# Performance work log

Measured on AMD Instinct MI355X. Metric: run time of the kernel, lower is better.

The kernel has to match this reference:

```python
import jax, jax.numpy as jnp
import numpy as np

NQ = 8
DIM = 2 ** NQ  # 256
PAIRS = [(i, j) for i in range(NQ) for j in range(i + 1, NQ)]
CNOT = jnp.array([[1, 0, 0, 0], [0, 1, 0, 0], [0, 0, 0, 1], [0, 0, 1, 0]], jnp.complex64)


def rx(t):
    c = jnp.cos(t / 2).astype(jnp.complex64)
    s = (-1j * jnp.sin(t / 2)).astype(jnp.complex64)
    return jnp.stack([jnp.stack([c, s]), jnp.stack([s, c])])


def ry(t):
    c = jnp.cos(t / 2)
    s = jnp.sin(t / 2)
    return jnp.stack([jnp.stack([c, -s]), jnp.stack([s, c])]).astype(jnp.complex64)


def rz(t):
    e = jnp.exp(-1j * jnp.asarray(t, jnp.float32) / 2).astype(jnp.complex64)
    z = jnp.zeros((), jnp.complex64)
    return jnp.stack([jnp.stack([e, z]), jnp.stack([z, jnp.conj(e)])])


def ising_xx(phi):
    c = jnp.cos(phi / 2).astype(jnp.complex64)
    s = (-1j * jnp.sin(phi / 2)).astype(jnp.complex64)
    z = jnp.zeros((), jnp.complex64)
    return jnp.stack([
        jnp.stack([c, z, z, s]),
        jnp.stack([z, c, s, z]),
        jnp.stack([z, s, c, z]),
        jnp.stack([s, z, z, c]),
    ])


def apply_u(rho, U, wires):
    """rho: (2,)*16 tensor (8 ket axes, 8 bra axes). Apply U rho U^dagger on wires."""
    k = len(wires)
    Ut = U.reshape((2,) * (2 * k))
    rho = jnp.tensordot(Ut, rho, axes=(tuple(range(k, 2 * k)), tuple(wires)))
    rho = jnp.moveaxis(rho, tuple(range(k)), tuple(wires))
    bra = tuple(w + NQ for w in wires)
    rho = jnp.tensordot(jnp.conj(Ut), rho, axes=(tuple(range(k, 2 * k)), bra))
    rho = jnp.moveaxis(rho, tuple(range(k)), bra)
    return rho


def conv_block(rho, b1, b2, p):
    rho = apply_u(rho, rz(-jnp.pi / 2), (b2,))
    rho = apply_u(rho, CNOT, (b2, b1))
    rho = apply_u(rho, rz(p[0]), (b1,))
    rho = apply_u(rho, ry(p[1]), (b2,))
    rho = apply_u(rho, CNOT, (b1, b2))
    rho = apply_u(rho, ry(p[2]), (b2,))
    rho = apply_u(rho, CNOT, (b2, b1))
    rho = apply_u(rho, rz(jnp.pi / 2), (b1,))
    return rho


def pool_block(rho, b1, b2, p):
    rho = apply_u(rho, rz(-jnp.pi / 2), (b2,))
    rho = apply_u(rho, CNOT, (b2, b1))
    rho = apply_u(rho, rz(p[0]), (b1,))
    rho = apply_u(rho, ry(p[1]), (b2,))
    rho = apply_u(rho, CNOT, (b1, b2))
    rho = apply_u(rho, ry(p[2]), (b2,))
    return rho


def quantum_fusion_layer(x, weights, coupling, p_flip):
    # AmplitudeEmbedding with normalize=True -> pure state, then rho = |psi><psi|
    psi = (x / jnp.sqrt(jnp.sum(x * x))).astype(jnp.complex64)
    rho = jnp.outer(psi, jnp.conj(psi)).reshape((2,) * (2 * NQ))
    X = jnp.array([[0, 1], [1, 0]], jnp.complex64)
    for i in range(NQ):
        rho = apply_u(rho, rx(weights[i]), (i,))
        rho = apply_u(rho, ry(weights[i + NQ]), (i,))
        rho = apply_u(rho, rz(weights[i + 2 * NQ]), (i,))
        if p_flip > 0.0:  # BitFlip channel; identity when p=0
            rho = (1.0 - p_flip) * rho + p_flip * apply_u(rho, X, (i,))
    for (i, j) in PAIRS:
        rho = apply_u(rho, ising_xx(coupling[i, j]), (i, j))
    # data-dependent adjacency -> blend (equivalent to conditional apply for adj in {0,1})
    cmin = coupling.min()
    cmax = coupling.max()
    adj = ((coupling - cmin) / (cmax - cmin)) > 0.5
    count = jnp.zeros((), jnp.int32)
    for (i, j) in PAIRS:
        a = adj[i, j]
        idx = 3 * NQ + 6 * count
        p6 = jax.lax.dynamic_slice(weights, (idx,), (6,))
        r2 = conv_block(rho, i, j, p6[:3])
        r2 = pool_block(r2, i, j, p6[3:])
        af = a.astype(jnp.float32)
        rho = af * r2 + (1.0 - af) * rho
        count = count + a.astype(jnp.int32)
    return rho.reshape(DIM, DIM)


def setup_inputs() -> dict:
    key = jax.random.key(0)
    k1, k2, k3 = jax.random.split(key, 3)
    x = jax.random.uniform(k1, (DIM,), dtype=jnp.float32)
    weights = jax.random.uniform(k2, (210,), dtype=jnp.float32)
    coupling = jax.random.uniform(k3, (NQ, NQ), dtype=jnp.float32)
    return {"x": x, "weights": weights, "coupling": coupling}


def reference(x, weights, coupling):
    # forward returns the noiseless state (noise_strength=0); the noisy run is only printed
    return quantum_fusion_layer(x, weights, coupling, 0.0)
```

## Files before the change

kernel.cpp:

```cpp
#include <hip/hip_runtime.h>

#define RHALF 0.70710678118654752440f

struct St { float vr[4]; float vi[4]; int lane; };

static __device__ __forceinline__ void phase_mul(float& ar, float& ai, float c, float s) {
    float nr = c*ar - s*ai;
    float ni = c*ai + s*ar;
    ar = nr; ai = ni;
}

static __device__ __forceinline__ void xxupd(float& ar, float& ai, float pr, float pi, float c, float s) {
    ar = c*ar + s*pi;
    ai = c*ai - s*pr;
}

static __device__ __forceinline__ void rx_pair(float& ar, float& ai, float& br, float& bi, float c, float s) {
    float nar = c*ar + s*bi, nai = c*ai - s*br;
    float nbr = c*br + s*ai, nbi = c*bi - s*ar;
    ar=nar; ai=nai; br=nbr; bi=nbi;
}

static __device__ __forceinline__ void ry_pair(float& ar, float& ai, float& br, float& bi, float c, float s) {
    float nar = c*ar - s*br, nai = c*ai - s*bi;
    float nbr = s*ar + c*br, nbi = s*ai + c*bi;
    ar=nar; ai=nai; br=nbr; bi=nbi;
}

static __device__ __forceinline__ void cswap2(float& ar, float& ai, float& br, float& bi, bool ctl) {
    float n0 = ctl ? br : ar, n1 = ctl ? ar : br;
    float m0 = ctl ? bi : ai, m1 = ctl ? ai : bi;
    ar = n0; br = n1; ai = m0; bi = m1;
}

static __device__ __forceinline__ void swapf(float& a, float& b) { float t=a; a=b; b=t; }

static __device__ __forceinline__ void xx2(float& ar,float& ai,float& br,float& bi,int lm,float c,float s) {
    float pbr = __shfl_xor(ar, lm, 64), pbi = __shfl_xor(ai, lm, 64);
    float par = __shfl_xor(br, lm, 64), pai = __shfl_xor(bi, lm, 64);
    xxupd(ar,ai,par,pai,c,s);
    xxupd(br,bi,pbr,pbi,c,s);
}


static __device__ __forceinline__ void gRZ(St& st, int q, float c, float s) {
    if (q == 0) {
        phase_mul(st.vr[0],st.vi[0],c,-s); phase_mul(st.vr[1],st.vi[1],c,-s);
        phase_mul(st.vr[2],st.vi[2],c, s); phase_mul(st.vr[3],st.vi[3],c, s);
    } else if (q == 1) {
        phase_mul(st.vr[0],st.vi[0],c,-s); phase_mul(st.vr[2],st.vi[2],c,-s);
        phase_mul(st.vr[1],st.vi[1],c, s); phase_mul(st.vr[3],st.vi[3],c, s);
    } else {
        int ml = 1 << (7-q);
        float sg = (st.lane & ml) ? s : -s;
        phase_mul(st.vr[0],st.vi[0],c,sg);
        phase_mul(st.vr[1],st.vi[1],c,sg);
        phase_mul(st.vr[2],st.vi[2],c,sg);
        phase_mul(st.vr[3],st.vi[3],c,sg);
    }
}

static __device__ __forceinline__ void gRX(St& st, int q, float c, float s) {
    if (q == 0) {
        rx_pair(st.vr[0],st.vi[0],st.vr[2],st.vi[2],c,s);
        rx_pair(st.vr[1],st.vi[1],st.vr[3],st.vi[3],c,s);
    } else if (q == 1) {
        rx_pair(st.vr[0],st.vi[0],st.vr[1],st.vi[1],c,s);
        rx_pair(st.vr[2],st.vi[2],st.vr[3],st.vi[3],c,s);
    } else {
        int ml = 1 << (7-q);
        #pragma unroll
        for (int k=0;k<4;++k) {
            float pr = __shfl_xor(st.vr[k], ml, 64);
            float pi = __shfl_xor(st.vi[k], ml, 64);
            xxupd(st.vr[k], st.vi[k], pr, pi, c, s);
        }
    }
}

static __device__ __forceinline__ void gRY(St& st, int q, float c, float s) {
    if (q == 0) {
        ry_pair(st.vr[0],st.vi[0],st.vr[2],st.vi[2],c,s);
        ry_pair(st.vr[1],st.vi[1],st.vr[3],st.vi[3],c,s);
    } else if (q == 1) {
        ry_pair(st.vr[0],st.vi[0],st.vr[1],st.vi[1],c,s);
        ry_pair(st.vr[2],st.vi[2],st.vr[3],st.vi[3],c,s);
    } else {
        int ml = 1 << (7-q);
        float pc = (st.lane & ml) ? s : -s;
        #pragma unroll
        for (int k=0;k<4;++k) {
            float pr = __shfl_xor(st.vr[k], ml, 64);
            float pi = __shfl_xor(st.vi[k], ml, 64);
            st.vr[k] = c*st.vr[k] + pc*pr;
            st.vi[k] = c*st.vi[k] + pc*pi;
        }
    }
}

static __device__ __forceinline__ void gCNOT(St& st, int qc, int qt) {
    if (qc <= 1 && qt <= 1) {
        if (qc == 0) { swapf(st.vr[2],st.vr[3]); swapf(st.vi[2],st.vi[3]); }
        else         { swapf(st.vr[1],st.vr[3]); swapf(st.vi[1],st.vi[3]); }
    } else if (qc <= 1) {
        int ml = 1 << (7-qt);
        if (qc == 0) {
            st.vr[2]=__shfl_xor(st.vr[2],ml,64); st.vi[2]=__shfl_xor(st.vi[2],ml,64);
            st.vr[3]=__shfl_xor(st.vr[3],ml,64); st.vi[3]=__shfl_xor(st.vi[3],ml,64);
        } else {
            st.vr[1]=__shfl_xor(st.vr[1],ml,64); st.vi[1]=__shfl_xor(st.vi[1],ml,64);
            st.vr[3]=__shfl_xor(st.vr[3],ml,64); st.vi[3]=__shfl_xor(st.vi[3],ml,64);
        }
    } else if (qt <= 1) {
        int mlc = 1 << (7-qc);
        bool ctl = (st.lane & mlc) != 0;
        if (qt == 0) {
            cswap2(st.vr[0],st.vi[0],st.vr[2],st.vi[2],ctl);
            cswap2(st.vr[1],st.vi[1],st.vr[3],st.vi[3],ctl);
        } else {
            cswap2(st.vr[0],st.vi[0],st.vr[1],st.vi[1],ctl);
            cswap2(st.vr[2],st.vi[2],st.vr[3],st.vi[3],ctl);
        }
    } else {
        int mlt = 1 << (7-qt);
        int mlc = 1 << (7-qc);
        bool ctl = (st.lane & mlc) != 0;
        #pragma unroll
        for (int k=0;k<4;++k) {
            float pr = __shfl_xor(st.vr[k], mlt, 64);
            float pi = __shfl_xor(st.vi[k], mlt, 64);
            st.vr[k] = ctl ? pr : st.vr[k];
            st.vi[k] = ctl ? pi : st.vi[k];
        }
    }
}

static __device__ __forceinline__ void gXX(St& st, int qa, int qb, float c, float s) {
    if (qb <= 1) {
        float p0r=st.vr[3],p0i=st.vi[3],p1r=st.vr[2],p1i=st.vi[2];
        float p2r=st.vr[1],p2i=st.vi[1],p3r=st.vr[0],p3i=st.vi[0];
        xxupd(st.vr[0],st.vi[0],p0r,p0i,c,s);
        xxupd(st.vr[1],st.vi[1],p1r,p1i,c,s);
        xxupd(st.vr[2],st.vi[2],p2r,p2i,c,s);
        xxupd(st.vr[3],st.vi[3],p3r,p3i,c,s);
    } else if (qa <= 1) {
        int lm = 1 << (7-qb);
        if (qa == 0) {
            xx2(st.vr[0],st.vi[0],st.vr[2],st.vi[2],lm,c,s);
            xx2(st.vr[1],st.vi[1],st.vr[3],st.vi[3],lm,c,s);
        } else {
            xx2(st.vr[0],st.vi[0],st.vr[1],st.vi[1],lm,c,s);
            xx2(st.vr[2],st.vi[2],st.vr[3],st.vi[3],lm,c,s);
        }
    } else {
        int lm = (1<<(7-qa)) | (1<<(7-qb));
        #pragma unroll
        for (int k=0;k<4;++k) {
            float pr = __shfl_xor(st.vr[k], lm, 64);
            float pi = __shfl_xor(st.vi[k], lm, 64);
            xxupd(st.vr[k],st.vi[k],pr,pi,c,s);
        }
    }
}

__global__ __launch_bounds__(64) void evolve_kernel(const float* __restrict__ x,
                                                    const float* __restrict__ w,
                                                    const float* __restrict__ cp,
                                                    float2* __restrict__ psi) {
    __shared__ float2 tw[256];
    __shared__ float2 tc[64];
    int lane = threadIdx.x;

    #pragma unroll
    for (int k=0;k<4;++k) {
        int idx = k*64 + lane;
        float a = (idx < 210) ? w[idx] : 0.0f;
        float sn, cn; sincosf(0.5f*a, &sn, &cn);
        tw[idx] = make_float2(cn, sn);
    }
    float cv = cp[lane];
    { float sn, cn; sincosf(0.5f*cv, &sn, &cn); tc[lane] = make_float2(cn, sn); }

    St st; st.lane = lane;
    float ss = 0.f;
    #pragma unroll
    for (int k=0;k<4;++k) {
        float xv = x[k*64 + lane];
        st.vr[k] = xv; st.vi[k] = 0.f;
        ss += xv*xv;
    }
    #pragma unroll
    for (int m=32;m>0;m>>=1) ss += __shfl_xor(ss, m, 64);
    float inv = 1.0f / sqrtf(ss);
    #pragma unroll
    for (int k=0;k<4;++k) st.vr[k] *= inv;

    float mn = cv, mx = cv;
    #pragma unroll
    for (int m=32;m>0;m>>=1) {
        mn = fminf(mn, __shfl_xor(mn, m, 64));
        mx = fmaxf(mx, __shfl_xor(mx, m, 64));
    }
    unsigned long long adj = __ballot(((cv - mn) / (mx - mn)) > 0.5f);

    __syncthreads();

    #pragma unroll
    for (int q=0;q<8;++q) {
        float2 cs;
        cs = tw[q];      gRX(st, q, cs.x, cs.y);
        cs = tw[q+8];    gRY(st, q, cs.x, cs.y);
        cs = tw[q+16];   gRZ(st, q, cs.x, cs.y);
    }

    #pragma unroll
    for (int i=0;i<8;++i) {
        #pragma unroll
        for (int j=i+1;j<8;++j) {
            float2 cs = tc[i*8+j];
            gXX(st, i, j, cs.x, cs.y);
        }
    }

    int count = 0;
    #pragma unroll
    for (int i=0;i<8;++i) {
        #pragma unroll
        for (int j=i+1;j<8;++j) {
            if ((adj >> (i*8 + j)) & 1ull) {
                int pb = 24 + 6*count;
                float2 cs;
                gRZ(st, j, RHALF, -RHALF);
                gCNOT(st, j, i);
                cs = tw[pb+0]; gRZ(st, i, cs.x, cs.y);
                cs = tw[pb+1]; gRY(st, j, cs.x, cs.y);
                gCNOT(st, i, j);
                cs = tw[pb+2]; gRY(st, j, cs.x, cs.y);
                gCNOT(st, j, i);
                gRZ(st, i, RHALF, RHALF);
                gRZ(st, j, RHALF, -RHALF);
                gCNOT(st, j, i);
                cs = tw[pb+3]; gRZ(st, i, cs.x, cs.y);
                cs = tw[pb+4]; gRY(st, j, cs.x, cs.y);
                gCNOT(st, i, j);
                cs = tw[pb+5]; gRY(st, j, cs.x, cs.y);
                ++count;
            }
        }
    }

    #pragma unroll
    for (int k=0;k<4;++k) psi[k*64+lane] = make_float2(st.vr[k], st.vi[k]);
}

__global__ __launch_bounds__(256) void outer_planar(const float2* __restrict__ psi,
                                                    float* __restrict__ out) {
    int c = threadIdx.x;
    int r = blockIdx.x;
    float2 pr = psi[r];
    float2 pc = psi[c];
    int idx = (r<<8) + c;
    out[idx]         = pr.x*pc.x + pr.y*pc.y;
    out[idx + 65536] = pr.y*pc.x - pr.x*pc.y;
}

__global__ __launch_bounds__(256) void outer_real(const float2* __restrict__ psi,
                                                  float* __restrict__ out) {
    int c = threadIdx.x;
    int r = blockIdx.x;
    float2 pr = psi[r];
    float2 pc = psi[c];
    out[(r<<8) + c] = pr.x*pc.x + pr.y*pc.y;
}

__global__ __launch_bounds__(256) void outer_interleaved(const float2* __restrict__ psi,
                                                         float2* __restrict__ out) {
    int c = threadIdx.x;
    int r = blockIdx.x;
    float2 pr = psi[r];
    float2 pc = psi[c];
    out[(r<<8) + c] = make_float2(pr.x*pc.x + pr.y*pc.y, pr.y*pc.x - pr.x*pc.y);
}

extern "C" void kernel_launch(void* const* d_in, const int* in_sizes, int n_in,
                              void* d_out, int out_size, void* d_ws, size_t ws_size,
                              hipStream_t stream) {
    (void)in_sizes; (void)n_in; (void)ws_size;
    const float* x  = (const float*)d_in[0];
    const float* w  = (const float*)d_in[1];
    const float* cp = (const float*)d_in[2];
    float2* psi = (float2*)d_ws;
    hipLaunchKernelGGL(evolve_kernel, dim3(1), dim3(64), 0, stream, x, w, cp, psi);
    if (out_size == 65536) {
        hipLaunchKernelGGL(outer_real, dim3(256), dim3(256), 0, stream, psi, (float*)d_out);
    } else if (out_size == 131072) {
        hipLaunchKernelGGL(outer_planar, dim3(256), dim3(256), 0, stream, psi, (float*)d_out);
    } else {
        hipLaunchKernelGGL(outer_interleaved, dim3(256), dim3(256), 0, stream, psi, (float2*)d_out);
    }
}
```

Measured before the change: 73.98 us.

## Precompute fused 4x4 two-qubit block unitaries and fused single-qubit gates

Each conditional conv+pool block, a sequence of CNOT, RZ and RY gates, is collapsed into one 4x4 complex matrix. The 28 lanes build these matrices in parallel and store them in shared memory, and the state is then updated with a single dense two-qubit apply per active pair. The RX, RY and RZ layers on each qubit are likewise fused into one 2x2 unitary. The IsingXX gates are reordered so that consecutive gates mix lanes differently. The goal is fewer sequential shuffle and gate steps on the single-wavefront critical path, at the cost of dense complex MACs and more shuffles per fused block.

Result: faster. 68.14 us (-7.9%).

```diff
diff --git a/kernel.cpp b/kernel.cpp
--- a/kernel.cpp
+++ b/kernel.cpp
@@ -2,38 +2,22 @@
 
 #define RHALF 0.70710678118654752440f
 
+typedef float2 cpx;
+
+static __device__ __forceinline__ cpx cmul(cpx a, cpx b) {
+    return make_float2(a.x*b.x - a.y*b.y, a.x*b.y + a.y*b.x);
+}
+static __device__ __forceinline__ void cmac(cpx& n, cpx k, cpx a) {
+    n.x += k.x*a.x - k.y*a.y;
+    n.y += k.x*a.y + k.y*a.x;
+}
+
 struct St { float vr[4]; float vi[4]; int lane; };
-
-static __device__ __forceinline__ void phase_mul(float& ar, float& ai, float c, float s) {
-    float nr = c*ar - s*ai;
-    float ni = c*ai + s*ar;
-    ar = nr; ai = ni;
-}
 
 static __device__ __forceinline__ void xxupd(float& ar, float& ai, float pr, float pi, float c, float s) {
     ar = c*ar + s*pi;
     ai = c*ai - s*pr;
 }
-
-static __device__ __forceinline__ void rx_pair(float& ar, float& ai, float& br, float& bi, float c, float s) {
-    float nar = c*ar + s*bi, nai = c*ai - s*br;
-    float nbr = c*br + s*ai, nbi = c*bi - s*ar;
-    ar=nar; ai=nai; br=nbr; bi=nbi;
-}
-
-static __device__ __forceinline__ void ry_pair(float& ar, float& ai, float& br, float& bi, float c, float s) {
-    float nar = c*ar - s*br, nai = c*ai - s*bi;
-    float nbr = s*ar + c*br, nbi = s*ai + c*bi;
-    ar=nar; ai=nai; br=nbr; bi=nbi;
-}
-
-static __device__ __forceinline__ void cswap2(float& ar, float& ai, float& br, float& bi, bool ctl) {
-    float n0 = ctl ? br : ar, n1 = ctl ? ar : br;
-    float m0 = ctl ? bi : ai, m1 = ctl ? ai : bi;
-    ar = n0; br = n1; ai = m0; bi = m1;
-}
-
-static __device__ __forceinline__ void swapf(float& a, float& b) { float t=a; a=b; b=t; }
 
 static __device__ __forceinline__ void xx2(float& ar,float& ai,float& br,float& bi,int lm,float c,float s) {
     float pbr = __shfl_xor(ar, lm, 64), pbi = __shfl_xor(ai, lm, 64);
@@ -42,98 +26,6 @@
     xxupd(br,bi,pbr,pbi,c,s);
 }
 
-
-static __device__ __forceinline__ void gRZ(St& st, int q, float c, float s) {
-    if (q == 0) {
-        phase_mul(st.vr[0],st.vi[0],c,-s); phase_mul(st.vr[1],st.vi[1],c,-s);
-        phase_mul(st.vr[2],st.vi[2],c, s); phase_mul(st.vr[3],st.vi[3],c, s);
-    } else if (q == 1) {
-        phase_mul(st.vr[0],st.vi[0],c,-s); phase_mul(st.vr[2],st.vi[2],c,-s);
-        phase_mul(st.vr[1],st.vi[1],c, s); phase_mul(st.vr[3],st.vi[3],c, s);
-    } else {
-        int ml = 1 << (7-q);
-        float sg = (st.lane & ml) ? s : -s;
-        phase_mul(st.vr[0],st.vi[0],c,sg);
-        phase_mul(st.vr[1],st.vi[1],c,sg);
-        phase_mul(st.vr[2],st.vi[2],c,sg);
-        phase_mul(st.vr[3],st.vi[3],c,sg);
-    }
-}
-
-static __device__ __forceinline__ void gRX(St& st, int q, float c, float s) {
-    if (q == 0) {
-        rx_pair(st.vr[0],st.vi[0],st.vr[2],st.vi[2],c,s);
-        rx_pair(st.vr[1],st.vi[1],st.vr[3],st.vi[3],c,s);
-    } else if (q == 1) {
-        rx_pair(st.vr[0],st.vi[0],st.vr[1],st.vi[1],c,s);
-        rx_pair(st.vr[2],st.vi[2],st.vr[3],st.vi[3],c,s);
-    } else {
-        int ml = 1 << (7-q);
-        #pragma unroll
-        for (int k=0;k<4;++k) {
-            float pr = __shfl_xor(st.vr[k], ml, 64);
-            float pi = __shfl_xor(st.vi[k], ml, 64);
-            xxupd(st.vr[k], st.vi[k], pr, pi, c, s);
-        }
-    }
-}
-
-static __device__ __forceinline__ void gRY(St& st, int q, float c, float s) {
-    if (q == 0) {
-        ry_pair(st.vr[0],st.vi[0],st.vr[2],st.vi[2],c,s);
-        ry_pair(st.vr[1],st.vi[1],st.vr[3],st.vi[3],c,s);
-    } else if (q == 1) {
-        ry_pair(st.vr[0],st.vi[0],st.vr[1],st.vi[1],c,s);
-        ry_pair(st.vr[2],st.vi[2],st.vr[3],st.vi[3],c,s);
-    } else {
-        int ml = 1 << (7-q);
-        float pc = (st.lane & ml) ? s : -s;
-        #pragma unroll
-        for (int k=0;k<4;++k) {
-            float pr = __shfl_xor(st.vr[k], ml, 64);
-            float pi = __shfl_xor(st.vi[k], ml, 64);
-            st.vr[k] = c*st.vr[k] + pc*pr;
-            st.vi[k] = c*st.vi[k] + pc*pi;
-        }
-    }
-}
-
-static __device__ __forceinline__ void gCNOT(St& st, int qc, int qt) {
-    if (qc <= 1 && qt <= 1) {
-        if (qc == 0) { swapf(st.vr[2],st.vr[3]); swapf(st.vi[2],st.vi[3]); }
-        else         { swapf(st.vr[1],st.vr[3]); swapf(st.vi[1],st.vi[3]); }
-    } else if (qc <= 1) {
-        int ml = 1 << (7-qt);
-        if (qc == 0) {
-            st.vr[2]=__shfl_xor(st.vr[2],ml,64); st.vi[2]=__shfl_xor(st.vi[2],ml,64);
-            st.vr[3]=__shfl_xor(st.vr[3],ml,64); st.vi[3]=__shfl_xor(st.vi[3],ml,64);
-        } else {
-            st.vr[1]=__shfl_xor(st.vr[1],ml,64); st.vi[1]=__shfl_xor(st.vi[1],ml,64);
-            st.vr[3]=__shfl_xor(st.vr[3],ml,64); st.vi[3]=__shfl_xor(st.vi[3],ml,64);
-        }
-    } else if (qt <= 1) {
-        int mlc = 1 << (7-qc);
-        bool ctl = (st.lane & mlc) != 0;
-        if (qt == 0) {
-            cswap2(st.vr[0],st.vi[0],st.vr[2],st.vi[2],ctl);
-            cswap2(st.vr[1],st.vi[1],st.vr[3],st.vi[3],ctl);
-        } else {
-            cswap2(st.vr[0],st.vi[0],st.vr[1],st.vi[1],ctl);
-            cswap2(st.vr[2],st.vi[2],st.vr[3],st.vi[3],ctl);
-        }
-    } else {
-        int mlt = 1 << (7-qt);
-        int mlc = 1 << (7-qc);
-        bool ctl = (st.lane & mlc) != 0;
-        #pragma unroll
-        for (int k=0;k<4;++k) {
-            float pr = __shfl_xor(st.vr[k], mlt, 64);
-            float pi = __shfl_xor(st.vi[k], mlt, 64);
-            st.vr[k] = ctl ? pr : st.vr[k];
-            st.vi[k] = ctl ? pi : st.vi[k];
-        }
-    }
-}
 
 static __device__ __forceinline__ void gXX(St& st, int qa, int qb, float c, float s) {
     if (qb <= 1) {
@@ -163,23 +55,77 @@
     }
 }
 
+
+static __device__ __forceinline__ void applyBlockLL(St& st, const cpx* bm, int p, int i, int j) {
+    int mi = 1 << (7-i), mj = 1 << (7-j);
+    int r = ((st.lane & mi) ? 2 : 0) | ((st.lane & mj) ? 1 : 0);
+    const cpx* row = bm + p*16 + r*4;
+    cpx K0 = row[r], K1 = row[r^1], K2 = row[r^2], K3 = row[r^3];
+    #pragma unroll
+    for (int k=0;k<4;++k) {
+        float p1r = __shfl_xor(st.vr[k], mj, 64),    p1i = __shfl_xor(st.vi[k], mj, 64);
+        float p2r = __shfl_xor(st.vr[k], mi, 64),    p2i = __shfl_xor(st.vi[k], mi, 64);
+        float p3r = __shfl_xor(st.vr[k], mi|mj, 64), p3i = __shfl_xor(st.vi[k], mi|mj, 64);
+        cpx n = make_float2(0.f,0.f);
+        cmac(n, K0, make_float2(st.vr[k], st.vi[k]));
+        cmac(n, K1, make_float2(p1r,p1i));
+        cmac(n, K2, make_float2(p2r,p2i));
+        cmac(n, K3, make_float2(p3r,p3i));
+        st.vr[k] = n.x; st.vi[k] = n.y;
+    }
+}
+
+static __device__ __forceinline__ void applyBlockMixed(St& st, const cpx* bm, int p, int i, int j) {
+    int mj = 1 << (7-j);
+    int bj = (st.lane & mj) ? 1 : 0;
+    const cpx* base = bm + p*16;
+    cpx lo0 = base[bj*4+0], lo1 = base[bj*4+1], lo2 = base[bj*4+2], lo3 = base[bj*4+3];
+    cpx hi0 = base[(2+bj)*4+0], hi1 = base[(2+bj)*4+1], hi2 = base[(2+bj)*4+2], hi3 = base[(2+bj)*4+3];
+    cpx lo_o0 = bj ? lo1 : lo0;  cpx lo_s0 = bj ? lo0 : lo1;
+    cpx lo_o1 = bj ? lo3 : lo2;  cpx lo_s1 = bj ? lo2 : lo3;
+    cpx hi_o0 = bj ? hi1 : hi0;  cpx hi_s0 = bj ? hi0 : hi1;
+    cpx hi_o1 = bj ? hi3 : hi2;  cpx hi_s1 = bj ? hi2 : hi3;
+    float sr[4], si[4];
+    #pragma unroll
+    for (int k=0;k<4;++k) { sr[k] = __shfl_xor(st.vr[k], mj, 64); si[k] = __shfl_xor(st.vi[k], mj, 64); }
+    int ri = (i==0) ? 2 : 1;
+    #pragma unroll
+    for (int t=0; t<2; ++t) {
+        int k0 = (i==0) ? t : (t*2);
+        int k1 = k0 | ri;
+        cpx a0 = make_float2(st.vr[k0], st.vi[k0]);
+        cpx a1 = make_float2(st.vr[k1], st.vi[k1]);
+        cpx s0 = make_float2(sr[k0], si[k0]);
+        cpx s1 = make_float2(sr[k1], si[k1]);
+        cpx n0 = make_float2(0.f,0.f), n1 = make_float2(0.f,0.f);
+        cmac(n0, lo_o0, a0); cmac(n0, lo_s0, s0); cmac(n0, lo_o1, a1); cmac(n0, lo_s1, s1);
+        cmac(n1, hi_o0, a0); cmac(n1, hi_s0, s0); cmac(n1, hi_o1, a1); cmac(n1, hi_s1, s1);
+        st.vr[k0]=n0.x; st.vi[k0]=n0.y; st.vr[k1]=n1.x; st.vi[k1]=n1.y;
+    }
+}
+
+static __device__ __forceinline__ void applyBlock01(St& st, const cpx* bm, int p) {
+    const cpx* base = bm + p*16;
+    cpx a[4];
+    #pragma unroll
+    for (int k=0;k<4;++k) a[k] = make_float2(st.vr[k], st.vi[k]);
+    #pragma unroll
+    for (int r=0;r<4;++r) {
+        cpx n = make_float2(0.f,0.f);
+        #pragma unroll
+        for (int c=0;c<4;++c) cmac(n, base[r*4+c], a[c]);
+        st.vr[r]=n.x; st.vi[r]=n.y;
+    }
+}
+
 __global__ __launch_bounds__(64) void evolve_kernel(const float* __restrict__ x,
                                                     const float* __restrict__ w,
                                                     const float* __restrict__ cp,
                                                     float2* __restrict__ psi) {
-    __shared__ float2 tw[256];
-    __shared__ float2 tc[64];
+    __shared__ cpx tc[64];
+    __shared__ cpx u1[32];
+    __shared__ cpx bmat[28*16];
     int lane = threadIdx.x;
-
-    #pragma unroll
-    for (int k=0;k<4;++k) {
-        int idx = k*64 + lane;
-        float a = (idx < 210) ? w[idx] : 0.0f;
-        float sn, cn; sincosf(0.5f*a, &sn, &cn);
-        tw[idx] = make_float2(cn, sn);
-    }
-    float cv = cp[lane];
-    { float sn, cn; sincosf(0.5f*cv, &sn, &cn); tc[lane] = make_float2(cn, sn); }
 
     St st; st.lane = lane;
     float ss = 0.f;
@@ -195,56 +141,148 @@
     #pragma unroll
     for (int k=0;k<4;++k) st.vr[k] *= inv;
 
+    float cv = cp[lane];
+    { float sn, cn; sincosf(0.5f*cv, &sn, &cn); tc[lane] = make_float2(cn, sn); }
     float mn = cv, mx = cv;
     #pragma unroll
     for (int m=32;m>0;m>>=1) {
         mn = fminf(mn, __shfl_xor(mn, m, 64));
         mx = fmaxf(mx, __shfl_xor(mx, m, 64));
     }
-    unsigned long long adj = __ballot(((cv - mn) / (mx - mn)) > 0.5f);
+    unsigned long long adj64 = __ballot(((cv - mn) / (mx - mn)) > 0.5f);
+
+    int ii = 0, jj = 0;
+    if (lane < 28) {
+        int rem = lane;
+        while (rem >= 7-ii) { rem -= 7-ii; ++ii; }
+        jj = ii + 1 + rem;
+    }
+    unsigned int f = (lane < 28) ? (unsigned int)((adj64 >> (ii*8 + jj)) & 1ull) : 0u;
+    unsigned long long pmw = __ballot(f != 0u);
+    unsigned int pm = (unsigned int)(pmw & 0xFFFFFFFull);
+    int prefix = __popcll(pmw & ((1ull << lane) - 1ull));
+
+    {
+        int q = lane & 7;
+        float sn0,cn0,sn1,cn1,sn2,cn2;
+        sincosf(0.5f*w[q],    &sn0, &cn0);
+        sincosf(0.5f*w[q+8],  &sn1, &cn1);
+        sincosf(0.5f*w[q+16], &sn2, &cn2);
+        cpx A00 = make_float2( cn1*cn0,  sn1*sn0);
+        cpx A01 = make_float2(-sn1*cn0, -cn1*sn0);
+        cpx A10 = make_float2( sn1*cn0, -cn1*sn0);
+        cpx A11 = make_float2( cn1*cn0, -sn1*sn0);
+        cpx e0 = make_float2(cn2,-sn2), e1 = make_float2(cn2, sn2);
+        if (lane < 8) {
+            u1[q*4+0] = cmul(e0,A00); u1[q*4+1] = cmul(e0,A01);
+            u1[q*4+2] = cmul(e1,A10); u1[q*4+3] = cmul(e1,A11);
+        }
+    }
+
+    if (lane < 28) {
+        int idx = 24 + 6*prefix;
+        float s0,c0,s1,c1,s2,c2,s3,c3,s4,c4,s5,c5;
+        sincosf(0.5f*w[idx+0], &s0, &c0);
+        sincosf(0.5f*w[idx+1], &s1, &c1);
+        sincosf(0.5f*w[idx+2], &s2, &c2);
+        sincosf(0.5f*w[idx+3], &s3, &c3);
+        sincosf(0.5f*w[idx+4], &s4, &c4);
+        sincosf(0.5f*w[idx+5], &s5, &c5);
+        cpx m[16];
+        #pragma unroll
+        for (int e=0;e<16;++e) m[e] = make_float2(0.f,0.f);
+        m[0]  = make_float2(RHALF,  RHALF);
+        m[5]  = make_float2(RHALF, -RHALF);
+        m[10] = make_float2(RHALF,  RHALF);
+        m[15] = make_float2(RHALF, -RHALF);
+        #define RSWAP(a,b) { _Pragma("unroll") for (int c_=0;c_<4;++c_){ cpx t_=m[(a)*4+c_]; m[(a)*4+c_]=m[(b)*4+c_]; m[(b)*4+c_]=t_; } }
+        #define DIAG_I(e0x,e0y,e1x,e1y) { cpx ea_=make_float2(e0x,e0y), eb_=make_float2(e1x,e1y); \
+            _Pragma("unroll") for (int e_=0;e_<8;++e_)  m[e_]   = cmul(ea_, m[e_]); \
+            _Pragma("unroll") for (int e_=8;e_<16;++e_) m[e_]   = cmul(eb_, m[e_]); }
+        #define DIAG_J(e0x,e0y,e1x,e1y) { cpx ea_=make_float2(e0x,e0y), eb_=make_float2(e1x,e1y); \
+            _Pragma("unroll") for (int c_=0;c_<4;++c_){ m[c_]=cmul(ea_,m[c_]); m[8+c_]=cmul(ea_,m[8+c_]); \
+                                                        m[4+c_]=cmul(eb_,m[4+c_]); m[12+c_]=cmul(eb_,m[12+c_]); } }
+        #define RY_J(cc,sc) { _Pragma("unroll") for (int c_=0;c_<4;++c_){ \
+            cpx a_=m[c_],   b_=m[4+c_];  m[c_]  =make_float2((cc)*a_.x-(sc)*b_.x,(cc)*a_.y-(sc)*b_.y); \
+                                         m[4+c_]=make_float2((sc)*a_.x+(cc)*b_.x,(sc)*a_.y+(cc)*b_.y); \
+            cpx d_=m[8+c_], e_=m[12+c_]; m[8+c_] =make_float2((cc)*d_.x-(sc)*e_.x,(cc)*d_.y-(sc)*e_.y); \
+                                         m[12+c_]=make_float2((sc)*d_.x+(cc)*e_.x,(sc)*d_.y+(cc)*e_.y); } }
+        RSWAP(1,3)
+        DIAG_I(c0,-s0, c0, s0)
+        RY_J(c1,s1)
+        RSWAP(2,3)
+        RY_J(c2,s2)
+        RSWAP(1,3)
+        DIAG_I(RHALF,-RHALF, RHALF,RHALF)
+        DIAG_J(RHALF,RHALF, RHALF,-RHALF)
+        RSWAP(1,3)
+        DIAG_I(c3,-s3, c3, s3)
+        RY_J(c4,s4)
+        RSWAP(2,3)
+        RY_J(c5,s5)
+        #pragma unroll
+        for (int e=0;e<16;++e) bmat[lane*16+e] = m[e];
+        #undef RSWAP
+        #undef DIAG_I
+        #undef DIAG_J
+        #undef RY_J
+    }
 
     __syncthreads();
 
     #pragma unroll
     for (int q=0;q<8;++q) {
-        float2 cs;
-        cs = tw[q];      gRX(st, q, cs.x, cs.y);
-        cs = tw[q+8];    gRY(st, q, cs.x, cs.y);
-        cs = tw[q+16];   gRZ(st, q, cs.x, cs.y);
-    }
-
-    #pragma unroll
-    for (int i=0;i<8;++i) {
-        #pragma unroll
-        for (int j=i+1;j<8;++j) {
-            float2 cs = tc[i*8+j];
-            gXX(st, i, j, cs.x, cs.y);
-        }
-    }
-
-    int count = 0;
-    #pragma unroll
-    for (int i=0;i<8;++i) {
-        #pragma unroll
-        for (int j=i+1;j<8;++j) {
-            if ((adj >> (i*8 + j)) & 1ull) {
-                int pb = 24 + 6*count;
-                float2 cs;
-                gRZ(st, j, RHALF, -RHALF);
-                gCNOT(st, j, i);
-                cs = tw[pb+0]; gRZ(st, i, cs.x, cs.y);
-                cs = tw[pb+1]; gRY(st, j, cs.x, cs.y);
-                gCNOT(st, i, j);
-                cs = tw[pb+2]; gRY(st, j, cs.x, cs.y);
-                gCNOT(st, j, i);
-                gRZ(st, i, RHALF, RHALF);
-                gRZ(st, j, RHALF, -RHALF);
-                gCNOT(st, j, i);
-                cs = tw[pb+3]; gRZ(st, i, cs.x, cs.y);
-                cs = tw[pb+4]; gRY(st, j, cs.x, cs.y);
-                gCNOT(st, i, j);
-                cs = tw[pb+5]; gRY(st, j, cs.x, cs.y);
-                ++count;
+        cpx U00=u1[q*4+0], U01=u1[q*4+1], U10=u1[q*4+2], U11=u1[q*4+3];
+        if (q >= 2) {
+            int ml = 1 << (7-q);
+            bool hi = (lane & ml) != 0;
+            cpx A = hi ? U11 : U00;
+            cpx B = hi ? U10 : U01;
+            #pragma unroll
+            for (int k=0;k<4;++k) {
+                float pr = __shfl_xor(st.vr[k], ml, 64);
+                float pi = __shfl_xor(st.vi[k], ml, 64);
+                cpx n = make_float2(0.f,0.f);
+                cmac(n, A, make_float2(st.vr[k], st.vi[k]));
+                cmac(n, B, make_float2(pr, pi));
+                st.vr[k]=n.x; st.vi[k]=n.y;
+            }
+        } else {
+            int ri = (q==0) ? 2 : 1;
+            #pragma unroll
+            for (int t=0;t<2;++t) {
+                int k0 = (q==0) ? t : (t*2);
+                int k1 = k0 | ri;
+                cpx a = make_float2(st.vr[k0], st.vi[k0]);
+                cpx b = make_float2(st.vr[k1], st.vi[k1]);
+                cpx n0 = make_float2(0.f,0.f), n1 = make_float2(0.f,0.f);
+                cmac(n0, U00, a); cmac(n0, U01, b);
+                cmac(n1, U10, a); cmac(n1, U11, b);
+                st.vr[k0]=n0.x; st.vi[k0]=n0.y; st.vr[k1]=n1.x; st.vi[k1]=n1.y;
+            }
+        }
+    }
+
+    {
+        constexpr int XI[28] = {0,1,2,3, 1,0,3,4, 2,1,0,5, 3,2,1,0, 4,3,2,0, 5,4,0,1, 6,0,1,2};
+        constexpr int XJ[28] = {7,6,5,4, 7,2,6,5, 7,3,4,6, 7,4,5,6, 7,5,6,1, 7,6,3,2, 7,5,4,3};
+        #pragma unroll
+        for (int g=0; g<28; ++g) {
+            cpx cs = tc[XI[g]*8 + XJ[g]];
+            gXX(st, XI[g], XJ[g], cs.x, cs.y);
+        }
+    }
+
+    {
+        constexpr int PI3[28] = {0,0,0,0,0,0,0, 1,1,1,1,1,1, 2,2,2,2,2, 3,3,3,3, 4,4,4, 5,5, 6};
+        constexpr int PJ3[28] = {1,2,3,4,5,6,7, 2,3,4,5,6,7, 3,4,5,6,7, 4,5,6,7, 5,6,7, 6,7, 7};
+        #pragma unroll
+        for (int p=0;p<28;++p) {
+            if ((pm >> p) & 1u) {
+                const int i = PI3[p], j = PJ3[p];
+                if (i >= 2)      applyBlockLL(st, bmat, p, i, j);
+                else if (j >= 2) applyBlockMixed(st, bmat, p, i, j);
+                else             applyBlock01(st, bmat, p);
             }
         }
     }
```
